# Kernel optimization log

Hardware: AMD Instinct MI355X
Metric: run time of the kernel (lower is better)

The kernel has to match this reference:

```python
import jax, jax.numpy as jnp
import numpy as np


def setup_inputs() -> dict:
    key = jax.random.key(0)
    k1, k2, k3, k4 = jax.random.split(key, 4)
    B, S, dAR, dEnc, K, N = 32, 128, 256, 256, 12, 128
    W = S - K  # windowSize = 116
    cFeature = jax.random.normal(k1, (B, S, dAR), dtype=jnp.float32)
    encodedData = jax.random.normal(k2, (B, S, dEnc), dtype=jnp.float32)
    Wp = jax.random.normal(k3, (K, dEnc, dAR), dtype=jnp.float32) * 0.05
    extIdx = jax.random.randint(k4, (N * W * B,), 0, B * S, dtype=jnp.int64)
    return {"cFeature": cFeature, "encodedData": encodedData, "Wp": Wp, "extIdx": extIdx}


def reference(cFeature, encodedData, Wp, extIdx):
    B, S, dAR = cFeature.shape
    K = Wp.shape[0]                      # nPredicts
    e = encodedData.shape[-1]            # dimOutputEncoder
    W = S - K                            # windowSize
    N = extIdx.shape[0] // (B * W)       # negativeSamplingExt

    c = cFeature[:, :W]                                          # (B, W, dAR)
    # negative sampling: flat gather then reshape, as in sample()
    negExt = encodedData.reshape(-1, e)[extIdx].reshape(B, N, W, e)

    # all predictor Linears at once: locC[k] = c @ Wp[k].T -> (K, B, W, e)
    locC = jnp.einsum('bwa,kea->kbwe', c, Wp)

    # positive sequences: encodedData[:, k+1 : k+1+W] for each predictor k
    pos = jnp.stack([encodedData[:, k + 1:k + 1 + W] for k in range(K)])  # (K,B,W,e)

    inv_e = 1.0 / e  # (locC * cand).mean(dim=3)
    posScore = jnp.einsum('kbwe,kbwe->kbw', locC, pos) * inv_e            # (K,B,W)
    negScore = jnp.einsum('kbwe,bnwe->kbnw', locC, negExt) * inv_e        # (K,B,N,W)

    logits = jnp.concatenate([posScore[:, :, None, :], negScore], axis=2)  # (K,B,1+N,W)
    logits = jnp.transpose(logits, (0, 1, 3, 2)).reshape(K, B * W, 1 + N)

    # cross-entropy with label 0 (positive is class 0), mean over B*W samples
    lse = jax.nn.logsumexp(logits, axis=-1)                                # (K, B*W)
    losses = jnp.mean(lse - logits[..., 0], axis=-1)                       # (K,)
    acc = jnp.mean((jnp.argmax(logits, axis=-1) == 0).astype(jnp.float32), axis=-1)
    return losses[None, :], acc[None, :]
```

## Files before the change

### kernel.cpp

```cpp
#include <hip/hip_runtime.h>

#define HD __device__ __forceinline__

typedef __attribute__((ext_vector_type(4))) float f32x4;
typedef __attribute__((ext_vector_type(8))) short bf16x8;

constexpr int B_ = 32, S_ = 128, DA = 256, DE = 256, K_ = 12, N_ = 128;
constexpr int W_ = S_ - K_;
constexpr int BW = B_ * W_;
constexpr int NC = 144;

HD unsigned short f2bf(float f) {
    unsigned u = __float_as_uint(f);
    u += 0x7fffu + ((u >> 16) & 1u);
    return (unsigned short)(u >> 16);
}
HD float bf2f(unsigned short h) { return __uint_as_float(((unsigned)h) << 16); }

__global__ void k_detect(const unsigned int* __restrict__ idx, unsigned int* __restrict__ flag) {
    __shared__ int anyNZ;
    if (threadIdx.x == 0) anyNZ = 0;
    __syncthreads();
    int nz = 0;
    for (int i = threadIdx.x; i < 4096; i += 256) nz |= (idx[2 * i + 1] != 0u);
    if (nz) atomicOr(&anyNZ, 1);
    __syncthreads();
    if (threadIdx.x == 0) *flag = (anyNZ == 0) ? 1u : 0u;
}

__global__ void k_cast(const float* __restrict__ in, unsigned short* __restrict__ out, int n4) {
    int i = blockIdx.x * 256 + threadIdx.x;
    if (i >= n4) return;
    float4 v = ((const float4*)in)[i];
    ushort4 o;
    o.x = f2bf(v.x); o.y = f2bf(v.y); o.z = f2bf(v.z); o.w = f2bf(v.w);
    ((ushort4*)out)[i] = o;
}

__global__ __launch_bounds__(256) void k_locc(const unsigned short* __restrict__ Abf,
                                              const unsigned short* __restrict__ Wpbf,
                                              unsigned short* __restrict__ locC) {
    int bx = blockIdx.x;
    int k  = bx / 58;
    int r  = bx % 58;
    int mt = r >> 1;
    int et = r & 1;

    __shared__ unsigned short As[128][40];
    __shared__ unsigned short Bs[128][40];

    int tid  = threadIdx.x;
    int lane = tid & 63;
    int wid  = tid >> 6;
    int wr   = wid >> 1, wc = wid & 1;
    int l15  = lane & 15, lk = lane >> 4;

    f32x4 acc[4][4] = {};

    int srow = tid >> 1, spart = tid & 1;
    int m  = mt * 128 + srow;
    int bb = m / W_, ww = m - bb * W_;
    const unsigned short* aSrc = Abf + ((bb * S_ + ww) * DA) + spart * 16;
    const unsigned short* bSrc = Wpbf + ((k * DE + et * 128 + srow) * DA) + spart * 16;

    for (int c = 0; c < 8; ++c) {
        uint4 av0 = ((const uint4*)(aSrc + c * 32))[0];
        uint4 av1 = ((const uint4*)(aSrc + c * 32))[1];
        uint4 bv0 = ((const uint4*)(bSrc + c * 32))[0];
        uint4 bv1 = ((const uint4*)(bSrc + c * 32))[1];
        __syncthreads();
        ((uint4*)&As[srow][spart * 16])[0]     = av0;
        ((uint4*)&As[srow][spart * 16 + 8])[0] = av1;
        ((uint4*)&Bs[srow][spart * 16])[0]     = bv0;
        ((uint4*)&Bs[srow][spart * 16 + 8])[0] = bv1;
        __syncthreads();
        bf16x8 af[4], bfv[4];
        #pragma unroll
        for (int f = 0; f < 4; ++f) {
            af[f]  = *(const bf16x8*)&As[wr * 64 + f * 16 + l15][lk * 8];
            bfv[f] = *(const bf16x8*)&Bs[wc * 64 + f * 16 + l15][lk * 8];
        }
        #pragma unroll
        for (int fi = 0; fi < 4; ++fi)
            #pragma unroll
            for (int fj = 0; fj < 4; ++fj)
                acc[fi][fj] = __builtin_amdgcn_mfma_f32_16x16x32_bf16(af[fi], bfv[fj], acc[fi][fj], 0, 0, 0);
    }

    #pragma unroll
    for (int fi = 0; fi < 4; ++fi) {
        #pragma unroll
        for (int fj = 0; fj < 4; ++fj) {
            f32x4 v = acc[fi][fj];
            int eOut = et * 128 + wc * 64 + fj * 16 + l15;
            #pragma unroll
            for (int rr = 0; rr < 4; ++rr) {
                int mOut = mt * 128 + wr * 64 + fi * 16 + lk * 4 + rr;
                locC[(mOut * K_ + k) * DE + eOut] = f2bf(v[rr]);
            }
        }
    }
}

__global__ __launch_bounds__(256) void k_score(const unsigned short* __restrict__ Ebf,
                                               const unsigned int* __restrict__ idxRaw,
                                               const unsigned short* __restrict__ locC,
                                               const unsigned int* __restrict__ flag,
                                               float* __restrict__ partial) {
    __shared__ float smat[K_][NC + 4];

    int tid  = threadIdx.x;
    int lane = tid & 63;
    int wid  = tid >> 6;
    int l15  = lane & 15, lk = lane >> 4;
    int p    = blockIdx.x;
    int b    = p / W_, w = p - b * W_;

    bool i64 = (*flag != 0u);

    bf16x8 af[8];
    const unsigned short* aBase = locC + ((size_t)p * K_ + l15) * DE + lk * 8;
    #pragma unroll
    for (int ks = 0; ks < 8; ++ks) {
        bf16x8 a = {};
        if (l15 < K_) a = *(const bf16x8*)(aBase + ks * 32);
        af[ks] = a;
    }

    int nnf = (wid == 0) ? 3 : 2;
    int nfl[3] = { wid, wid + 4, 8 };

    constexpr float inv_e = 1.0f / 256.0f;

    for (int q = 0; q < nnf; ++q) {
        int nf  = nfl[q];
        int row = nf * 16 + l15;
        int erow;
        if (row < N_) {
            int fi = (b * N_ + row) * W_ + w;
            erow = i64 ? (int)idxRaw[2 * fi] : (int)idxRaw[fi];
        } else {
            int j = row - N_;
            erow = b * S_ + ((j < K_) ? (w + j + 1) : 0);
        }
        const unsigned short* bBase = Ebf + (size_t)erow * DE + lk * 8;

        f32x4 acc = {};
        #pragma unroll
        for (int ks = 0; ks < 8; ++ks) {
            bf16x8 bfv = *(const bf16x8*)(bBase + ks * 32);
            acc = __builtin_amdgcn_mfma_f32_16x16x32_bf16(af[ks], bfv, acc, 0, 0, 0);
        }
        if (lk < 3) {
            #pragma unroll
            for (int rr = 0; rr < 4; ++rr)
                smat[lk * 4 + rr][nf * 16 + l15] = acc[rr] * inv_e;
        }
    }
    __syncthreads();

    for (int kk = 0; kk < 3; ++kk) {
        int k = wid * 3 + kk;
        float v0 = smat[k][lane], v1 = smat[k][lane + 64];
        float mx = fmaxf(v0, v1);
        #pragma unroll
        for (int off = 32; off > 0; off >>= 1) mx = fmaxf(mx, __shfl_xor(mx, off));
        float ps = smat[k][N_ + k];
        float M  = fmaxf(mx, ps);
        float se = __expf(v0 - M) + __expf(v1 - M);
        #pragma unroll
        for (int off = 32; off > 0; off >>= 1) se += __shfl_xor(se, off);
        se += __expf(ps - M);
        if (lane == 0) {
            partial[p * 24 + k]      = M + __logf(se) - ps;
            partial[p * 24 + 12 + k] = (ps >= mx) ? 1.0f : 0.0f;
        }
    }
}

__global__ void k_reduce(const float* __restrict__ partial, float* __restrict__ out) {
    int o = blockIdx.x;
    float s = 0.f;
    for (int pp = threadIdx.x; pp < BW; pp += 256) s += partial[pp * 24 + o];
    #pragma unroll
    for (int off = 32; off > 0; off >>= 1) s += __shfl_xor(s, off);
    __shared__ float w4[4];
    if ((threadIdx.x & 63) == 0) w4[threadIdx.x >> 6] = s;
    __syncthreads();
    if (threadIdx.x == 0)
        out[o] = (w4[0] + w4[1] + w4[2] + w4[3]) * (1.0f / BW);
}

extern "C" void kernel_launch(void* const* d_in, const int* in_sizes, int n_in,
                              void* d_out, int out_size, void* d_ws, size_t ws_size,
                              hipStream_t stream) {
    const float* cFeat = (const float*)d_in[0];
    const float* E     = (const float*)d_in[1];
    const float* Wp    = (const float*)d_in[2];
    const unsigned int* idxRaw = (const unsigned int*)d_in[3];

    char* ws = (char*)d_ws;
    unsigned short* locC    = (unsigned short*)(ws);
    unsigned short* Abf     = (unsigned short*)(ws + 22806528);
    unsigned short* Wpbf    = (unsigned short*)(ws + 24903680);
    float*          partial = (float*)        (ws + 26476544);
    unsigned int*   flag    = (unsigned int*) (ws + 26832896);
    unsigned short* Ebf     = (unsigned short*)(ws + 26833024);

    k_detect<<<1, 256, 0, stream>>>(idxRaw, flag);
    k_cast<<<(B_ * S_ * DA / 4 + 255) / 256, 256, 0, stream>>>(cFeat, Abf, B_ * S_ * DA / 4);
    k_cast<<<(K_ * DE * DA / 4 + 255) / 256, 256, 0, stream>>>(Wp, Wpbf, K_ * DE * DA / 4);
    k_cast<<<(B_ * S_ * DE / 4 + 255) / 256, 256, 0, stream>>>(E, Ebf, B_ * S_ * DE / 4);
    k_locc<<<12 * 58, 256, 0, stream>>>(Abf, Wpbf, locC);
    k_score<<<BW, 256, 0, stream>>>(Ebf, idxRaw, locC, flag, partial);
    k_reduce<<<24, 256, 0, stream>>>(partial, (float*)d_out);
}
```

Before: 137.3 us.

## Fuse cast/detect kernels and give each score position its own wave with register softmax

The three bf16 cast kernels and the index-width detection kernel become one launch, with the block index selecting which job a block does. The score kernel now gives each wavefront one (b,w) position. A wave gathers all 9 column fragments and runs the max, log-sum-exp and accuracy reductions in registers with intra-16-lane shuffles, so the shared-memory score matrix and the block barrier are gone. Partial results are stored k-major so the final reduction reads contiguous memory. In exchange each wave holds more accumulators and indices in registers, which may lower occupancy.

```diff
diff --git a/kernel.cpp b/kernel.cpp
--- a/kernel.cpp
+++ b/kernel.cpp
@@ -8,33 +8,38 @@
 constexpr int B_ = 32, S_ = 128, DA = 256, DE = 256, K_ = 12, N_ = 128;
 constexpr int W_ = S_ - K_;
 constexpr int BW = B_ * W_;
-constexpr int NC = 144;
 
 HD unsigned short f2bf(float f) {
     unsigned u = __float_as_uint(f);
     u += 0x7fffu + ((u >> 16) & 1u);
     return (unsigned short)(u >> 16);
 }
-HD float bf2f(unsigned short h) { return __uint_as_float(((unsigned)h) << 16); }
-
-__global__ void k_detect(const unsigned int* __restrict__ idx, unsigned int* __restrict__ flag) {
-    __shared__ int anyNZ;
-    if (threadIdx.x == 0) anyNZ = 0;
-    __syncthreads();
-    int nz = 0;
-    for (int i = threadIdx.x; i < 4096; i += 256) nz |= (idx[2 * i + 1] != 0u);
-    if (nz) atomicOr(&anyNZ, 1);
-    __syncthreads();
-    if (threadIdx.x == 0) *flag = (anyNZ == 0) ? 1u : 0u;
-}
-
-__global__ void k_cast(const float* __restrict__ in, unsigned short* __restrict__ out, int n4) {
-    int i = blockIdx.x * 256 + threadIdx.x;
-    if (i >= n4) return;
-    float4 v = ((const float4*)in)[i];
+
+__global__ void k_prep(const float* __restrict__ A, const float* __restrict__ Wp,
+                       const float* __restrict__ E, const unsigned int* __restrict__ idx,
+                       unsigned short* __restrict__ Abf, unsigned short* __restrict__ Wpbf,
+                       unsigned short* __restrict__ Ebf, unsigned int* __restrict__ flag) {
+    int bx = blockIdx.x;
+    const float* src; unsigned short* dst; int base;
+    if (bx < 1024)      { src = A;  dst = Abf;  base = bx; }
+    else if (bx < 1792) { src = Wp; dst = Wpbf; base = bx - 1024; }
+    else if (bx < 2816) { src = E;  dst = Ebf;  base = bx - 1792; }
+    else {
+        __shared__ int anyNZ;
+        if (threadIdx.x == 0) anyNZ = 0;
+        __syncthreads();
+        int nz = 0;
+        for (int i = threadIdx.x; i < 4096; i += 256) nz |= (idx[2 * i + 1] != 0u);
+        if (nz) atomicOr(&anyNZ, 1);
+        __syncthreads();
+        if (threadIdx.x == 0) *flag = (anyNZ == 0) ? 1u : 0u;
+        return;
+    }
+    int i = base * 256 + threadIdx.x;
+    float4 v = ((const float4*)src)[i];
     ushort4 o;
     o.x = f2bf(v.x); o.y = f2bf(v.y); o.z = f2bf(v.z); o.w = f2bf(v.w);
-    ((ushort4*)out)[i] = o;
+    ((ushort4*)dst)[i] = o;
 }
 
 __global__ __launch_bounds__(256) void k_locc(const unsigned short* __restrict__ Abf,
@@ -107,16 +112,27 @@
                                                const unsigned short* __restrict__ locC,
                                                const unsigned int* __restrict__ flag,
                                                float* __restrict__ partial) {
-    __shared__ float smat[K_][NC + 4];
-
     int tid  = threadIdx.x;
     int lane = tid & 63;
     int wid  = tid >> 6;
     int l15  = lane & 15, lk = lane >> 4;
-    int p    = blockIdx.x;
+    int p    = blockIdx.x * 4 + wid;
     int b    = p / W_, w = p - b * W_;
 
     bool i64 = (*flag != 0u);
+
+    int rows[9];
+    #pragma unroll
+    for (int nf = 0; nf < 9; ++nf) {
+        int col = nf * 16 + l15;
+        if (col < N_) {
+            int fi = (b * N_ + col) * W_ + w;
+            rows[nf] = i64 ? (int)idxRaw[2 * fi] : (int)idxRaw[fi];
+        } else {
+            int j = col - N_;
+            rows[nf] = b * S_ + ((j < K_) ? (w + j + 1) : 0);
+        }
+    }
 
     bf16x8 af[8];
     const unsigned short* aBase = locC + ((size_t)p * K_ + l15) * DE + lk * 8;
@@ -127,53 +143,58 @@
         af[ks] = a;
     }
 
-    int nnf = (wid == 0) ? 3 : 2;
-    int nfl[3] = { wid, wid + 4, 8 };
-
-    constexpr float inv_e = 1.0f / 256.0f;
-
-    for (int q = 0; q < nnf; ++q) {
-        int nf  = nfl[q];
-        int row = nf * 16 + l15;
-        int erow;
-        if (row < N_) {
-            int fi = (b * N_ + row) * W_ + w;
-            erow = i64 ? (int)idxRaw[2 * fi] : (int)idxRaw[fi];
-        } else {
-            int j = row - N_;
-            erow = b * S_ + ((j < K_) ? (w + j + 1) : 0);
-        }
-        const unsigned short* bBase = Ebf + (size_t)erow * DE + lk * 8;
-
+    f32x4 accs[9];
+    #pragma unroll
+    for (int nf = 0; nf < 9; ++nf) {
+        const unsigned short* bBase = Ebf + (size_t)rows[nf] * DE + lk * 8;
         f32x4 acc = {};
         #pragma unroll
         for (int ks = 0; ks < 8; ++ks) {
             bf16x8 bfv = *(const bf16x8*)(bBase + ks * 32);
             acc = __builtin_amdgcn_mfma_f32_16x16x32_bf16(af[ks], bfv, acc, 0, 0, 0);
         }
-        if (lk < 3) {
-            #pragma unroll
-            for (int rr = 0; rr < 4; ++rr)
-                smat[lk * 4 + rr][nf * 16 + l15] = acc[rr] * inv_e;
-        }
-    }
-    __syncthreads();
-
-    for (int kk = 0; kk < 3; ++kk) {
-        int k = wid * 3 + kk;
-        float v0 = smat[k][lane], v1 = smat[k][lane + 64];
-        float mx = fmaxf(v0, v1);
-        #pragma unroll
-        for (int off = 32; off > 0; off >>= 1) mx = fmaxf(mx, __shfl_xor(mx, off));
-        float ps = smat[k][N_ + k];
-        float M  = fmaxf(mx, ps);
-        float se = __expf(v0 - M) + __expf(v1 - M);
-        #pragma unroll
-        for (int off = 32; off > 0; off >>= 1) se += __shfl_xor(se, off);
-        se += __expf(ps - M);
-        if (lane == 0) {
-            partial[p * 24 + k]      = M + __logf(se) - ps;
-            partial[p * 24 + 12 + k] = (ps >= mx) ? 1.0f : 0.0f;
+        accs[nf] = acc;
+    }
+
+    constexpr float inv_e = 1.0f / 256.0f;
+
+    float m0[4], s0[4];
+    #pragma unroll
+    for (int rr = 0; rr < 4; ++rr) {
+        float mx = accs[0][rr];
+        #pragma unroll
+        for (int nf = 1; nf < 8; ++nf) mx = fmaxf(mx, accs[nf][rr]);
+        m0[rr] = mx;
+    }
+    #pragma unroll
+    for (int off = 1; off < 16; off <<= 1)
+        #pragma unroll
+        for (int rr = 0; rr < 4; ++rr) m0[rr] = fmaxf(m0[rr], __shfl_xor(m0[rr], off));
+
+    #pragma unroll
+    for (int rr = 0; rr < 4; ++rr) {
+        float s = 0.f;
+        #pragma unroll
+        for (int nf = 0; nf < 8; ++nf) s += __expf((accs[nf][rr] - m0[rr]) * inv_e);
+        s0[rr] = s;
+    }
+    #pragma unroll
+    for (int off = 1; off < 16; off <<= 1)
+        #pragma unroll
+        for (int rr = 0; rr < 4; ++rr) s0[rr] += __shfl_xor(s0[rr], off);
+
+    if (l15 < K_ && lk == (l15 >> 2)) {
+        int k = l15;
+        #pragma unroll
+        for (int rr = 0; rr < 4; ++rr) {
+            if ((k & 3) == rr) {
+                float ps   = accs[8][rr] * inv_e;
+                float mneg = m0[rr] * inv_e;
+                float M    = fmaxf(mneg, ps);
+                float tot  = s0[rr] * __expf(mneg - M) + __expf(ps - M);
+                partial[k * BW + p]        = M + __logf(tot) - ps;
+                partial[(12 + k) * BW + p] = (ps >= mneg) ? 1.0f : 0.0f;
+            }
         }
     }
 }
@@ -181,7 +202,7 @@
 __global__ void k_reduce(const float* __restrict__ partial, float* __restrict__ out) {
     int o = blockIdx.x;
     float s = 0.f;
-    for (int pp = threadIdx.x; pp < BW; pp += 256) s += partial[pp * 24 + o];
+    for (int i = threadIdx.x; i < BW; i += 256) s += partial[o * BW + i];
     #pragma unroll
     for (int off = 32; off > 0; off >>= 1) s += __shfl_xor(s, off);
     __shared__ float w4[4];
@@ -207,11 +228,8 @@
     unsigned int*   flag    = (unsigned int*) (ws + 26832896);
     unsigned short* Ebf     = (unsigned short*)(ws + 26833024);
 
-    k_detect<<<1, 256, 0, stream>>>(idxRaw, flag);
-    k_cast<<<(B_ * S_ * DA / 4 + 255) / 256, 256, 0, stream>>>(cFeat, Abf, B_ * S_ * DA / 4);
-    k_cast<<<(K_ * DE * DA / 4 + 255) / 256, 256, 0, stream>>>(Wp, Wpbf, K_ * DE * DA / 4);
-    k_cast<<<(B_ * S_ * DE / 4 + 255) / 256, 256, 0, stream>>>(E, Ebf, B_ * S_ * DE / 4);
+    k_prep<<<2817, 256, 0, stream>>>(cFeat, Wp, E, idxRaw, Abf, Wpbf, Ebf, flag);
     k_locc<<<12 * 58, 256, 0, stream>>>(Abf, Wpbf, locC);
-    k_score<<<BW, 256, 0, stream>>>(Ebf, idxRaw, locC, flag, partial);
+    k_score<<<BW / 4, 256, 0, stream>>>(Ebf, idxRaw, locC, flag, partial);
     k_reduce<<<24, 256, 0, stream>>>(partial, (float*)d_out);
 }
```

Result: faster. 126.7 us (-7.7%).
